# Kernel optimization log

Measured on AMD Instinct MI355X. Metric: run time of the kernel, lower is better.

Reference implementation:

```python
import jax, jax.numpy as jnp
import numpy as np

N, E, H = 4096, 32768, 8
D0, C1, C2, C3 = 256, 448, 384, 256
K, M, G = 4, 500, 2000
NEG = 0.2   # GATConv LeakyReLU negative slope
EPS = 1e-5  # LayerNorm eps


def _gat(x, src, dst, W, a_s, a_d, b, heads, out_ch, concat):
    # PyG GATConv (self-loops already appended to src/dst by caller).
    n = x.shape[0]
    xp = (x @ W).reshape(n, heads, out_ch)                 # [N,H,C]
    s = jnp.einsum('nhc,hc->nh', xp, a_s)                  # alpha_src per node
    d = jnp.einsum('nhc,hc->nh', xp, a_d)                  # alpha_dst per node
    e = jax.nn.leaky_relu(s[src] + d[dst], NEG)            # [E,H]
    m = jax.ops.segment_max(e, dst, num_segments=n)
    m = jnp.where(jnp.isfinite(m), m, 0.0)
    p = jnp.exp(e - m[dst])
    z = jax.ops.segment_sum(p, dst, num_segments=n)
    alpha = p / (z[dst] + 1e-16)                           # per-dst softmax
    out = jax.ops.segment_sum(alpha[:, :, None] * xp[src], dst, num_segments=n)
    out = out.reshape(n, heads * out_ch) if concat else out[:, 0, :]
    return out + b


def _ln(x, g, b):
    mu = x.mean(-1, keepdims=True)
    v = ((x - mu) ** 2).mean(-1, keepdims=True)
    return (x - mu) * jax.lax.rsqrt(v + EPS) * g + b


def setup_inputs() -> dict:
    key = jax.random.key(0)
    ks = jax.random.split(key, 20)
    sc = 0.05
    inp = {
        'x': jax.random.normal(ks[0], (N, D0), jnp.float32),
        'edge_index': jax.random.randint(ks[1], (2, E), 0, N, jnp.int32),
        'W1': jax.random.normal(ks[2], (D0, H * C1), jnp.float32) * sc,
        'as1': jax.random.normal(ks[3], (H, C1), jnp.float32) * sc,
        'ad1': jax.random.normal(ks[4], (H, C1), jnp.float32) * sc,
        'b1': jnp.zeros((H * C1,), jnp.float32),
        'g1': jnp.ones((H * C1,), jnp.float32),
        'be1': jnp.zeros((H * C1,), jnp.float32),
        'W2': jax.random.normal(ks[5], (H * C1, H * C2), jnp.float32) * sc,
        'as2': jax.random.normal(ks[6], (H, C2), jnp.float32) * sc,
        'ad2': jax.random.normal(ks[7], (H, C2), jnp.float32) * sc,
        'b2': jnp.zeros((H * C2,), jnp.float32),
        'g2': jnp.ones((H * C2,), jnp.float32),
        'be2': jnp.zeros((H * C2,), jnp.float32),
        'W3': jax.random.normal(ks[8], (H * C2, H * C3), jnp.float32) * sc,
        'as3': jax.random.normal(ks[9], (H, C3), jnp.float32) * sc,
        'ad3': jax.random.normal(ks[10], (H, C3), jnp.float32) * sc,
        'b3': jnp.zeros((H * C3,), jnp.float32),
        'g3': jnp.ones((H * C3,), jnp.float32),
        'be3': jnp.zeros((H * C3,), jnp.float32),
        'Wh': jax.random.normal(ks[11], (K, H * C3, M), jnp.float32) * sc,
        'ash': jax.random.normal(ks[12], (K, 1, M), jnp.float32) * sc,
        'adh': jax.random.normal(ks[13], (K, 1, M), jnp.float32) * sc,
        'bh': jnp.zeros((K, M), jnp.float32),
        'idx': jnp.arange(G, dtype=jnp.int32).reshape(K, M),
    }
    return inp


def reference(x, edge_index, W1, as1, ad1, b1, g1, be1, W2, as2, ad2, b2, g2, be2,
              W3, as3, ad3, b3, g3, be3, Wh, ash, adh, bh, idx):
    n = x.shape[0]
    # eval mode: dropout_edge is identity; PyG GATConv adds self-loops
    loops = jnp.arange(n, dtype=edge_index.dtype)
    src = jnp.concatenate([edge_index[0], loops])
    dst = jnp.concatenate([edge_index[1], loops])

    h = jax.nn.relu(_gat(x, src, dst, W1, as1, ad1, b1, H, C1, True))
    h = _ln(h, g1, be1)
    h = jax.nn.relu(_gat(h, src, dst, W2, as2, ad2, b2, H, C2, True))
    h = _ln(h, g2, be2)
    h = jax.nn.relu(_gat(h, src, dst, W3, as3, ad3, b3, H, C3, True))
    h = _ln(h, g3, be3)

    per_head = jax.vmap(
        lambda Wk, ak_s, ak_d, bk: _gat(h, src, dst, Wk, ak_s, ak_d, bk, 1, M, False)
    )(Wh, ash, adh, bh)                                    # [K,N,M]

    vals = per_head.transpose(1, 0, 2).reshape(n, K * M)   # [N, G] in head order
    full = jnp.zeros((n, G), vals.dtype).at[:, idx.reshape(-1)].set(vals)
    return full, per_head
```

## Files before the change

### kernel.cpp

```cpp
#include <hip/hip_runtime.h>

#define NN 4096
#define EE 32768
#define ETOT (EE + NN)
#define HH 8
#define KK 4
#define MM 500
#define GG 2000
#define NEGS 0.2f
#define LNEPS 1e-5f

typedef unsigned short ushort;
typedef _Float16 half_t;
typedef __attribute__((ext_vector_type(8))) _Float16 half8;
typedef __attribute__((ext_vector_type(4))) _Float16 half4;
typedef __attribute__((ext_vector_type(4))) float floatx4;


__device__ __forceinline__ void get_edge(const int* __restrict__ ei, int e, int& s, int& d) {
    if (e < EE) { s = ei[e]; d = ei[EE + e]; }
    else        { s = e - EE; d = e - EE; }
}

__device__ __forceinline__ half_t f2h(float x) { return (half_t)x; }

__device__ __forceinline__ void async_lds16(const half_t* g, half_t* l) {
    __builtin_amdgcn_global_load_lds(
        (const __attribute__((address_space(1))) unsigned int*)(const void*)g,
        (__attribute__((address_space(3))) unsigned int*)(void*)l,
        16, 0, 0);
}


__global__ void k_count(const int* __restrict__ ei, int* deg) {
    int e = blockIdx.x * 256 + threadIdx.x;
    if (e < ETOT) { int s, d; get_edge(ei, e, s, d); atomicAdd(&deg[d], 1); }
}

__global__ void k_scan(const int* __restrict__ deg, int* rs, int n) {
    __shared__ int sums[1024];
    int tid = threadIdx.x;
    int base = tid * 4;
    int loc[4]; int s = 0;
    #pragma unroll
    for (int i = 0; i < 4; i++) {
        int v = (base + i < n) ? deg[base + i] : 0;
        loc[i] = s; s += v;
    }
    sums[tid] = s;
    __syncthreads();
    for (int off = 1; off < 1024; off <<= 1) {
        int v = (tid >= off) ? sums[tid - off] : 0;
        __syncthreads();
        sums[tid] += v;
        __syncthreads();
    }
    int prev = (tid > 0) ? sums[tid - 1] : 0;
    #pragma unroll
    for (int i = 0; i < 4; i++)
        if (base + i < n) rs[base + i] = prev + loc[i];
    if (tid == 1023) rs[n] = sums[1023];
}

__global__ void k_fill(const int* __restrict__ ei, const int* __restrict__ rs,
                       int* cur, int* csr_src) {
    int e = blockIdx.x * 256 + threadIdx.x;
    if (e < ETOT) {
        int s, d; get_edge(ei, e, s, d);
        int pos = rs[d] + atomicAdd(&cur[d], 1);
        csr_src[pos] = s;
    }
}


__global__ void k_f2h4(const floatx4* __restrict__ in, half4* __restrict__ out, int n4) {
    int i = blockIdx.x * 256 + threadIdx.x;
    if (i < n4) {
        floatx4 v = in[i];
        half4 o;
        o[0] = f2h(v[0]); o[1] = f2h(v[1]); o[2] = f2h(v[2]); o[3] = f2h(v[3]);
        out[i] = o;
    }
}


__global__ __launch_bounds__(256) void k_wt(const float* __restrict__ W,
                                            half_t* __restrict__ Wt,
                                            int Kd, int Nvalid, int ldw,
                                            long long sW, long long sWt) {
    __shared__ float t[32][33];
    const float* Wp = W + (size_t)blockIdx.z * sW;
    half_t* Wtp = Wt + (size_t)blockIdx.z * sWt;
    int n0 = blockIdx.x * 32, k0 = blockIdx.y * 32;
    int tx = threadIdx.x & 31, ty = threadIdx.x >> 5;
    #pragma unroll
    for (int i = 0; i < 32; i += 8)
        t[ty + i][tx] = (n0 + tx < Nvalid) ? Wp[(size_t)(k0 + ty + i) * ldw + n0 + tx] : 0.f;
    __syncthreads();
    #pragma unroll
    for (int i = 0; i < 32; i += 8)
        Wtp[(size_t)(n0 + ty + i) * Kd + k0 + tx] = f2h(t[tx][ty + i]);
}


#define BM 128
#define BN 128
#define BK 64

__global__ __launch_bounds__(256) void k_gemm_mfma(
    const half_t* __restrict__ A,
    const half_t* __restrict__ Bt,
    half_t* __restrict__ C,
    int Kd, int Nreal, int ldc,
    long long strideBt, long long strideC)
{
    __shared__ __align__(16) half_t As[BM * BK];
    __shared__ __align__(16) half_t Bs[BN * BK];

    const half_t* Btp = Bt + (size_t)blockIdx.z * strideBt;
    half_t* Cp = C + (size_t)blockIdx.z * strideC;
    int col0 = blockIdx.x * BN, row0 = blockIdx.y * BM;

    int lane = threadIdx.x & 63;
    int wave = threadIdx.x >> 6;
    int wm = (wave >> 1) * 64, wn = (wave & 1) * 64;

    int srow = wave * 32 + (lane >> 3);
    int gchunk = (lane & 7) ^ ((lane >> 3) & 7);
    const half_t* ga = A   + (size_t)(row0 + srow) * Kd + gchunk * 8;
    const half_t* gb = Btp + (size_t)(col0 + srow) * Kd + gchunk * 8;
    half_t* lA = &As[(wave * 32) * BK];
    half_t* lB = &Bs[(wave * 32) * BK];

    int r = lane & 15;
    int rx = r & 7;

    floatx4 acc[4][4];
    #pragma unroll
    for (int i = 0; i < 4; i++)
        #pragma unroll
        for (int j = 0; j < 4; j++) acc[i][j] = (floatx4){0.f, 0.f, 0.f, 0.f};

    for (int k0 = 0; k0 < Kd; k0 += BK) {
        #pragma unroll
        for (int j = 0; j < 4; j++) {
            async_lds16(ga + k0 + (size_t)(j * 8) * Kd, lA + (j * 8) * BK);
            async_lds16(gb + k0 + (size_t)(j * 8) * Kd, lB + (j * 8) * BK);
        }
        __syncthreads();
        #pragma unroll
        for (int kk = 0; kk < BK; kk += 32) {
            int phys = (((kk >> 3) + (lane >> 4)) ^ rx) << 3;
            half8 a[4], b[4];
            #pragma unroll
            for (int i = 0; i < 4; i++)
                a[i] = *(const half8*)&As[(wm + i * 16 + r) * BK + phys];
            #pragma unroll
            for (int j = 0; j < 4; j++)
                b[j] = *(const half8*)&Bs[(wn + j * 16 + r) * BK + phys];
            #pragma unroll
            for (int i = 0; i < 4; i++)
                #pragma unroll
                for (int j = 0; j < 4; j++)
                    acc[i][j] = __builtin_amdgcn_mfma_f32_16x16x32_f16(a[i], b[j], acc[i][j], 0, 0, 0);
        }
        __syncthreads();
    }

    int q4 = (lane >> 4) * 4;
    #pragma unroll
    for (int i = 0; i < 4; i++) {
        #pragma unroll
        for (int rr = 0; rr < 4; rr++) {
            int row = row0 + wm + i * 16 + q4 + rr;
            #pragma unroll
            for (int j = 0; j < 4; j++) {
                int col = col0 + wn + j * 16 + (lane & 15);
                if (col < Nreal) Cp[(size_t)row * ldc + col] = f2h(acc[i][j][rr]);
            }
        }
    }
}


__global__ void k_sd(const half_t* __restrict__ xp, const float* __restrict__ as_,
                     const float* __restrict__ ad_, float* s, float* d, int H, int C) {
    int n = blockIdx.x / H, h = blockIdx.x % H;
    int lane = threadIdx.x;
    const half4* row4 = (const half4*)(xp + (size_t)n * H * C + (size_t)h * C);
    const float* av = as_ + (size_t)h * C;
    const float* bv = ad_ + (size_t)h * C;
    int C4 = C >> 2;
    float ss = 0.f, dd = 0.f;
    for (int c4 = lane; c4 < C4; c4 += 64) {
        half4 v = row4[c4];
        floatx4 a = *(const floatx4*)(av + c4 * 4);
        floatx4 b = *(const floatx4*)(bv + c4 * 4);
        float x0 = (float)v[0], x1 = (float)v[1], x2 = (float)v[2], x3 = (float)v[3];
        ss += x0 * a[0] + x1 * a[1] + x2 * a[2] + x3 * a[3];
        dd += x0 * b[0] + x1 * b[1] + x2 * b[2] + x3 * b[3];
    }
    #pragma unroll
    for (int o = 32; o > 0; o >>= 1) {
        ss += __shfl_down(ss, o, 64);
        dd += __shfl_down(dd, o, 64);
    }
    if (lane == 0) { s[n * H + h] = ss; d[n * H + h] = dd; }
}


__global__ __launch_bounds__(256) void k_agg_ln(
    const half_t* __restrict__ xp, const float* __restrict__ s, const float* __restrict__ d,
    const int* __restrict__ csr_src, const int* __restrict__ rs,
    const float* __restrict__ bias, const float* __restrict__ gam,
    const float* __restrict__ bet, half_t* __restrict__ outh, int H, int C) {
    __shared__ int sh_src[256];
    __shared__ float sh_w[256 * HH];
    __shared__ float sh_d[HH];
    __shared__ float sh_z[HH];
    __shared__ float red[256];
    __shared__ float red2[256];
    int n = blockIdx.x, tid = threadIdx.x;
    int Dout = H * C;
    int NCH = Dout >> 3;
    int CCH = C >> 3;
    int start = rs[n], end = rs[n + 1];
    if (tid < H) { sh_d[tid] = d[(size_t)n * H + tid]; sh_z[tid] = 0.f; }
    float acc[2][8];
    #pragma unroll
    for (int a = 0; a < 2; a++)
        #pragma unroll
        for (int e = 0; e < 8; e++) acc[a][e] = 0.f;

    for (int e0 = start; e0 < end; e0 += 256) {
        int cnt = min(256, end - e0);
        if (tid < cnt) sh_src[tid] = csr_src[e0 + tid];
        __syncthreads();
        for (int i = tid; i < cnt * H; i += 256) {
            int ei = i / H, h = i - ei * H;
            float v = s[(size_t)sh_src[ei] * H + h] + sh_d[h];
            v = (v >= 0.f) ? v : NEGS * v;
            sh_w[i] = expf(v);
        }
        __syncthreads();
        if (tid < H) {
            float zz = 0.f;
            for (int i = 0; i < cnt; i++) zz += sh_w[i * H + tid];
            sh_z[tid] += zz;
        }
        int ai = 0;
        for (int ch = tid; ch < NCH; ch += 256, ai++) {
            int h = ch / CCH;
            float a0 = acc[ai][0], a1 = acc[ai][1], a2 = acc[ai][2], a3 = acc[ai][3];
            float a4 = acc[ai][4], a5 = acc[ai][5], a6 = acc[ai][6], a7 = acc[ai][7];
            for (int i = 0; i < cnt; i++) {
                float w = sh_w[i * H + h];
                half8 v = *(const half8*)(xp + (size_t)sh_src[i] * Dout + (ch << 3));
                a0 += w * (float)v[0]; a1 += w * (float)v[1];
                a2 += w * (float)v[2]; a3 += w * (float)v[3];
                a4 += w * (float)v[4]; a5 += w * (float)v[5];
                a6 += w * (float)v[6]; a7 += w * (float)v[7];
            }
            acc[ai][0] = a0; acc[ai][1] = a1; acc[ai][2] = a2; acc[ai][3] = a3;
            acc[ai][4] = a4; acc[ai][5] = a5; acc[ai][6] = a6; acc[ai][7] = a7;
        }
        __syncthreads();
    }

    float vals[2][8];
    float sum = 0.f, sumsq = 0.f;
    int ai = 0;
    for (int ch = tid; ch < NCH; ch += 256, ai++) {
        int h = ch / CCH;
        float zi = 1.f / (sh_z[h] + 1e-16f);
        #pragma unroll
        for (int e = 0; e < 8; e++) {
            float v = acc[ai][e] * zi + bias[(ch << 3) + e];
            v = fmaxf(v, 0.f);
            vals[ai][e] = v;
            sum += v; sumsq += v * v;
        }
    }
    red[tid] = sum; red2[tid] = sumsq;
    __syncthreads();
    for (int o = 128; o > 0; o >>= 1) {
        if (tid < o) { red[tid] += red[tid + o]; red2[tid] += red2[tid + o]; }
        __syncthreads();
    }
    float mu = red[0] / Dout;
    float var = red2[0] / Dout - mu * mu;
    float rstd = rsqrtf(var + LNEPS);
    ai = 0;
    for (int ch = tid; ch < NCH; ch += 256, ai++) {
        half8 o;
        #pragma unroll
        for (int e = 0; e < 8; e++)
            o[e] = f2h((vals[ai][e] - mu) * rstd * gam[(ch << 3) + e] + bet[(ch << 3) + e]);
        *(half8*)(outh + (size_t)n * Dout + (ch << 3)) = o;
    }
}


__global__ __launch_bounds__(256) void k_agg_head(
    const half_t* __restrict__ xp, const float* __restrict__ s, const float* __restrict__ d,
    const int* __restrict__ csr_src, const int* __restrict__ rs,
    const float* __restrict__ bias, const int* __restrict__ idxm,
    float* out_full, float* out_ph) {
    __shared__ int sh_src[256];
    __shared__ float sh_w[256 * KK];
    __shared__ float sh_d[KK];
    __shared__ float sh_z[KK];
    int n = blockIdx.x, tid = threadIdx.x;
    const int Dout = KK * MM;
    const int NCH = Dout >> 3;
    int start = rs[n], end = rs[n + 1];
    if (tid < KK) { sh_d[tid] = d[(size_t)n * KK + tid]; sh_z[tid] = 0.f; }
    float acc[8];
    #pragma unroll
    for (int e = 0; e < 8; e++) acc[e] = 0.f;
    int ch = tid;
    int cb = ch << 3;

    for (int e0 = start; e0 < end; e0 += 256) {
        int cnt = min(256, end - e0);
        if (tid < cnt) sh_src[tid] = csr_src[e0 + tid];
        __syncthreads();
        for (int i = tid; i < cnt * KK; i += 256) {
            int ei = i / KK, k = i - ei * KK;
            float v = s[(size_t)sh_src[ei] * KK + k] + sh_d[k];
            v = (v >= 0.f) ? v : NEGS * v;
            sh_w[i] = expf(v);
        }
        __syncthreads();
        if (tid < KK) {
            float zz = 0.f;
            for (int i = 0; i < cnt; i++) zz += sh_w[i * KK + tid];
            sh_z[tid] += zz;
        }
        if (ch < NCH) {
            for (int i = 0; i < cnt; i++) {
                const float* wv = &sh_w[i * KK];
                half8 v = *(const half8*)(xp + (size_t)sh_src[i] * Dout + cb);
                #pragma unroll
                for (int e = 0; e < 8; e++)
                    acc[e] += wv[(cb + e) / MM] * (float)v[e];
            }
        }
        __syncthreads();
    }
    if (ch < NCH) {
        #pragma unroll
        for (int e = 0; e < 8; e++) {
            int c = cb + e;
            int k = c / MM, m = c - k * MM;
            float v = acc[e] / (sh_z[k] + 1e-16f) + bias[c];
            out_ph[((size_t)k * NN + n) * MM + m] = v;
            out_full[(size_t)n * GG + idxm[c]] = v;
        }
    }
}


extern "C" void kernel_launch(void* const* d_in, const int* in_sizes, int n_in,
                              void* d_out, int out_size, void* d_ws, size_t ws_size,
                              hipStream_t stream) {
    (void)in_sizes; (void)n_in; (void)out_size; (void)ws_size;
    const float* x   = (const float*)d_in[0];
    const int*   ei  = (const int*)d_in[1];
    const float* W1  = (const float*)d_in[2];
    const float* as1 = (const float*)d_in[3];
    const float* ad1 = (const float*)d_in[4];
    const float* b1  = (const float*)d_in[5];
    const float* g1  = (const float*)d_in[6];
    const float* be1 = (const float*)d_in[7];
    const float* W2  = (const float*)d_in[8];
    const float* as2 = (const float*)d_in[9];
    const float* ad2 = (const float*)d_in[10];
    const float* b2  = (const float*)d_in[11];
    const float* g2  = (const float*)d_in[12];
    const float* be2 = (const float*)d_in[13];
    const float* W3  = (const float*)d_in[14];
    const float* as3 = (const float*)d_in[15];
    const float* ad3 = (const float*)d_in[16];
    const float* b3  = (const float*)d_in[17];
    const float* g3  = (const float*)d_in[18];
    const float* be3 = (const float*)d_in[19];
    const float* Wh  = (const float*)d_in[20];
    const float* ash = (const float*)d_in[21];
    const float* adh = (const float*)d_in[22];
    const float* bh  = (const float*)d_in[23];
    const int*   idxm = (const int*)d_in[24];
    float* out = (float*)d_out;

    char* w = (char*)d_ws;
    auto carve = [&](size_t bytes) { char* p = w; w += (bytes + 255) & ~(size_t)255; return p; };
    half_t* xp16    = (half_t*)carve((size_t)NN * 3584 * 2);
    half_t* Wt      = (half_t*)carve((size_t)3072 * 3584 * 2);
    float*  sarr    = (float*)carve((size_t)NN * HH * 4);
    float*  darr    = (float*)carve((size_t)NN * HH * 4);
    int*    csr_src = (int*)carve((size_t)ETOT * 4);
    int*    rowst   = (int*)carve((size_t)(NN + 1) * 4);
    int*    cur     = (int*)carve((size_t)NN * 4);
    half_t* Ah = (half_t*)d_out;

    hipMemsetAsync(cur, 0, (size_t)NN * 4, stream);
    k_count<<<(ETOT + 255) / 256, 256, 0, stream>>>(ei, cur);
    k_scan<<<1, 1024, 0, stream>>>(cur, rowst, NN);
    hipMemsetAsync(cur, 0, (size_t)NN * 4, stream);
    k_fill<<<(ETOT + 255) / 256, 256, 0, stream>>>(ei, rowst, cur, csr_src);

    k_f2h4<<<(NN * 64 + 255) / 256, 256, 0, stream>>>(
        (const floatx4*)x, (half4*)Ah, NN * 64);

    auto gat = [&](const float* W, const float* as_, const float* ad_,
                   const float* bias, const float* gam, const float* bet, int Din, int C) {
        int Dout = HH * C;
        k_wt<<<dim3(Dout / 32, Din / 32, 1), 256, 0, stream>>>(W, Wt, Din, Dout, Dout, 0, 0);
        k_gemm_mfma<<<dim3(Dout / BN, NN / BM, 1), 256, 0, stream>>>(
            Ah, Wt, xp16, Din, Dout, Dout, 0, 0);
        k_sd<<<NN * HH, 64, 0, stream>>>(xp16, as_, ad_, sarr, darr, HH, C);
        k_agg_ln<<<NN, 256, 0, stream>>>(xp16, sarr, darr, csr_src, rowst,
                                         bias, gam, bet, Ah, HH, C);
    };
    gat(W1, as1, ad1, b1, g1, be1, 256,  448);
    gat(W2, as2, ad2, b2, g2, be2, 3584, 384);
    gat(W3, as3, ad3, b3, g3, be3, 3072, 256);

    k_wt<<<dim3(512 / 32, 2048 / 32, KK), 256, 0, stream>>>(
        Wh, Wt, 2048, MM, MM, (long long)2048 * MM, (long long)512 * 2048);
    k_gemm_mfma<<<dim3(512 / BN, NN / BM, KK), 256, 0, stream>>>(
        Ah, Wt, xp16, 2048, MM, GG, (long long)512 * 2048, (long long)MM);
    k_sd<<<NN * KK, 64, 0, stream>>>(xp16, ash, adh, sarr, darr, KK, MM);
    k_agg_head<<<NN, 256, 0, stream>>>(xp16, sarr, darr, csr_src, rowst,
                                       bh, idxm, out, out + (size_t)NN * GG);
}
```

Baseline: 639.9 us.

## Fuse CSR fill with input cast, unroll gathers, use wave-shuffle LayerNorm reduction

The scan kernel now clears the degree counters itself, which removes one memset. The CSR fill and the fp32-to-fp16 input cast run in a single kernel, saving a launch. The aggregation kernels unroll the neighbor gather by four so more independent global loads are in flight, and the head kernel precomputes the per-element head index instead of dividing in the inner loop. The LayerNorm reduction changes from a shared-memory tree with many barriers to wave shuffles plus one barrier, which also changes the floating-point summation order slightly.

```diff
diff --git a/kernel.cpp b/kernel.cpp
--- a/kernel.cpp
+++ b/kernel.cpp
@@ -37,7 +37,7 @@
     if (e < ETOT) { int s, d; get_edge(ei, e, s, d); atomicAdd(&deg[d], 1); }
 }
 
-__global__ void k_scan(const int* __restrict__ deg, int* rs, int n) {
+__global__ void k_scan(int* deg, int* rs, int n) {
     __shared__ int sums[1024];
     int tid = threadIdx.x;
     int base = tid * 4;
@@ -47,6 +47,9 @@
         int v = (base + i < n) ? deg[base + i] : 0;
         loc[i] = s; s += v;
     }
+    #pragma unroll
+    for (int i = 0; i < 4; i++)
+        if (base + i < n) deg[base + i] = 0;
     sums[tid] = s;
     __syncthreads();
     for (int off = 1; off < 1024; off <<= 1) {
@@ -62,24 +65,20 @@
     if (tid == 1023) rs[n] = sums[1023];
 }
 
-__global__ void k_fill(const int* __restrict__ ei, const int* __restrict__ rs,
-                       int* cur, int* csr_src) {
-    int e = blockIdx.x * 256 + threadIdx.x;
-    if (e < ETOT) {
-        int s, d; get_edge(ei, e, s, d);
+__global__ void k_fill_f2h(const int* __restrict__ ei, const int* __restrict__ rs,
+                           int* cur, int* csr_src,
+                           const floatx4* __restrict__ x4, half4* __restrict__ xh4) {
+    int i = blockIdx.x * 256 + threadIdx.x;
+    if (i < ETOT) {
+        int s, d; get_edge(ei, i, s, d);
         int pos = rs[d] + atomicAdd(&cur[d], 1);
         csr_src[pos] = s;
     }
-}
-
-
-__global__ void k_f2h4(const floatx4* __restrict__ in, half4* __restrict__ out, int n4) {
-    int i = blockIdx.x * 256 + threadIdx.x;
-    if (i < n4) {
-        floatx4 v = in[i];
+    if (i < NN * 64) {
+        floatx4 v = x4[i];
         half4 o;
         o[0] = f2h(v[0]); o[1] = f2h(v[1]); o[2] = f2h(v[2]); o[3] = f2h(v[3]);
-        out[i] = o;
+        xh4[i] = o;
     }
 }
 
@@ -218,9 +217,10 @@
     __shared__ float sh_w[256 * HH];
     __shared__ float sh_d[HH];
     __shared__ float sh_z[HH];
-    __shared__ float red[256];
-    __shared__ float red2[256];
+    __shared__ float redm[4];
+    __shared__ float redv[4];
     int n = blockIdx.x, tid = threadIdx.x;
+    int lane = tid & 63, wv = tid >> 6;
     int Dout = H * C;
     int NCH = Dout >> 3;
     int CCH = C >> 3;
@@ -251,11 +251,29 @@
         int ai = 0;
         for (int ch = tid; ch < NCH; ch += 256, ai++) {
             int h = ch / CCH;
+            const half_t* base = xp + (ch << 3);
             float a0 = acc[ai][0], a1 = acc[ai][1], a2 = acc[ai][2], a3 = acc[ai][3];
             float a4 = acc[ai][4], a5 = acc[ai][5], a6 = acc[ai][6], a7 = acc[ai][7];
-            for (int i = 0; i < cnt; i++) {
+            int i = 0;
+            for (; i + 4 <= cnt; i += 4) {
+                half8 v0 = *(const half8*)(base + (size_t)sh_src[i + 0] * Dout);
+                half8 v1 = *(const half8*)(base + (size_t)sh_src[i + 1] * Dout);
+                half8 v2 = *(const half8*)(base + (size_t)sh_src[i + 2] * Dout);
+                half8 v3 = *(const half8*)(base + (size_t)sh_src[i + 3] * Dout);
+                float w0 = sh_w[(i + 0) * H + h], w1 = sh_w[(i + 1) * H + h];
+                float w2 = sh_w[(i + 2) * H + h], w3 = sh_w[(i + 3) * H + h];
+                a0 += w0 * (float)v0[0] + w1 * (float)v1[0] + w2 * (float)v2[0] + w3 * (float)v3[0];
+                a1 += w0 * (float)v0[1] + w1 * (float)v1[1] + w2 * (float)v2[1] + w3 * (float)v3[1];
+                a2 += w0 * (float)v0[2] + w1 * (float)v1[2] + w2 * (float)v2[2] + w3 * (float)v3[2];
+                a3 += w0 * (float)v0[3] + w1 * (float)v1[3] + w2 * (float)v2[3] + w3 * (float)v3[3];
+                a4 += w0 * (float)v0[4] + w1 * (float)v1[4] + w2 * (float)v2[4] + w3 * (float)v3[4];
+                a5 += w0 * (float)v0[5] + w1 * (float)v1[5] + w2 * (float)v2[5] + w3 * (float)v3[5];
+                a6 += w0 * (float)v0[6] + w1 * (float)v1[6] + w2 * (float)v2[6] + w3 * (float)v3[6];
+                a7 += w0 * (float)v0[7] + w1 * (float)v1[7] + w2 * (float)v2[7] + w3 * (float)v3[7];
+            }
+            for (; i < cnt; i++) {
+                half8 v = *(const half8*)(base + (size_t)sh_src[i] * Dout);
                 float w = sh_w[i * H + h];
-                half8 v = *(const half8*)(xp + (size_t)sh_src[i] * Dout + (ch << 3));
                 a0 += w * (float)v[0]; a1 += w * (float)v[1];
                 a2 += w * (float)v[2]; a3 += w * (float)v[3];
                 a4 += w * (float)v[4]; a5 += w * (float)v[5];
@@ -281,14 +299,17 @@
             sum += v; sumsq += v * v;
         }
     }
-    red[tid] = sum; red2[tid] = sumsq;
+    #pragma unroll
+    for (int o = 32; o > 0; o >>= 1) {
+        sum += __shfl_down(sum, o, 64);
+        sumsq += __shfl_down(sumsq, o, 64);
+    }
+    if (lane == 0) { redm[wv] = sum; redv[wv] = sumsq; }
     __syncthreads();
-    for (int o = 128; o > 0; o >>= 1) {
-        if (tid < o) { red[tid] += red[tid + o]; red2[tid] += red2[tid + o]; }
-        __syncthreads();
-    }
-    float mu = red[0] / Dout;
-    float var = red2[0] / Dout - mu * mu;
+    float tsum = redm[0] + redm[1] + redm[2] + redm[3];
+    float tsq  = redv[0] + redv[1] + redv[2] + redv[3];
+    float mu = tsum / Dout;
+    float var = tsq / Dout - mu * mu;
     float rstd = rsqrtf(var + LNEPS);
     ai = 0;
     for (int ch = tid; ch < NCH; ch += 256, ai++) {
@@ -320,6 +341,9 @@
     for (int e = 0; e < 8; e++) acc[e] = 0.f;
     int ch = tid;
     int cb = ch << 3;
+    int ke[8];
+    #pragma unroll
+    for (int e = 0; e < 8; e++) ke[e] = (cb + e) / MM;
 
     for (int e0 = start; e0 < end; e0 += 256) {
         int cnt = min(256, end - e0);
@@ -338,12 +362,28 @@
             sh_z[tid] += zz;
         }
         if (ch < NCH) {
-            for (int i = 0; i < cnt; i++) {
-                const float* wv = &sh_w[i * KK];
-                half8 v = *(const half8*)(xp + (size_t)sh_src[i] * Dout + cb);
+            const half_t* base = xp + cb;
+            int i = 0;
+            for (; i + 4 <= cnt; i += 4) {
+                half8 v0 = *(const half8*)(base + (size_t)sh_src[i + 0] * Dout);
+                half8 v1 = *(const half8*)(base + (size_t)sh_src[i + 1] * Dout);
+                half8 v2 = *(const half8*)(base + (size_t)sh_src[i + 2] * Dout);
+                half8 v3 = *(const half8*)(base + (size_t)sh_src[i + 3] * Dout);
+                const float* w0 = &sh_w[(i + 0) * KK];
+                const float* w1 = &sh_w[(i + 1) * KK];
+                const float* w2 = &sh_w[(i + 2) * KK];
+                const float* w3 = &sh_w[(i + 3) * KK];
                 #pragma unroll
                 for (int e = 0; e < 8; e++)
-                    acc[e] += wv[(cb + e) / MM] * (float)v[e];
+                    acc[e] += w0[ke[e]] * (float)v0[e] + w1[ke[e]] * (float)v1[e]
+                            + w2[ke[e]] * (float)v2[e] + w3[ke[e]] * (float)v3[e];
+            }
+            for (; i < cnt; i++) {
+                half8 v = *(const half8*)(base + (size_t)sh_src[i] * Dout);
+                const float* wvp = &sh_w[i * KK];
+                #pragma unroll
+                for (int e = 0; e < 8; e++)
+                    acc[e] += wvp[ke[e]] * (float)v[e];
             }
         }
         __syncthreads();
@@ -352,7 +392,7 @@
         #pragma unroll
         for (int e = 0; e < 8; e++) {
             int c = cb + e;
-            int k = c / MM, m = c - k * MM;
+            int k = ke[e], m = c - k * MM;
             float v = acc[e] / (sh_z[k] + 1e-16f) + bias[c];
             out_ph[((size_t)k * NN + n) * MM + m] = v;
             out_full[(size_t)n * GG + idxm[c]] = v;
@@ -406,11 +446,8 @@
     hipMemsetAsync(cur, 0, (size_t)NN * 4, stream);
     k_count<<<(ETOT + 255) / 256, 256, 0, stream>>>(ei, cur);
     k_scan<<<1, 1024, 0, stream>>>(cur, rowst, NN);
-    hipMemsetAsync(cur, 0, (size_t)NN * 4, stream);
-    k_fill<<<(ETOT + 255) / 256, 256, 0, stream>>>(ei, rowst, cur, csr_src);
-
-    k_f2h4<<<(NN * 64 + 255) / 256, 256, 0, stream>>>(
-        (const floatx4*)x, (half4*)Ah, NN * 64);
+    k_fill_f2h<<<(NN * 64 + 255) / 256, 256, 0, stream>>>(
+        ei, rowst, cur, csr_src, (const floatx4*)x, (half4*)Ah);
 
     auto gat = [&](const float* W, const float* as_, const float* ad_,
                    const float* bias, const float* gam, const float* bet, int Din, int C) {
```

After: 661.8 us. 1.03x slower.
